# Kernel optimization log

Measured on AMD Instinct MI355X. Metric: run time of the kernel, lower is better.

Reference implementation:

```python
import jax, jax.numpy as jnp
import numpy as np

B, S, H = 4, 1024, 2048
E = 16            # num_experts
K = 2             # num_experts_per_token
I = 1024          # per-expert intermediate_dim
N_SHARED = 2
I_SHARED = I * N_SHARED
RATIO = 0.1       # shared_expert_ratio
EPS = 1e-9


def _swiglu(x, wg, wu, wd):
    # SwiGLU, bias=False: down( silu(gate(x)) * up(x) )
    return (jax.nn.silu(x @ wg) * (x @ wu)) @ wd


def setup_inputs() -> dict:
    key = jax.random.key(0)
    ks = jax.random.split(key, 9)
    scale = 0.02
    x = jax.random.normal(ks[0], (B, S, H), dtype=jnp.float32)
    centroids = jax.random.normal(ks[1], (E, H), dtype=jnp.float32)  # nn.Parameter(randn)
    gate_bias = jnp.zeros((E,), dtype=jnp.float32)
    # shared expert SwiGLU weights (intermediate = I * n_shared_experts)
    wg_s = jax.random.normal(ks[2], (H, I_SHARED), dtype=jnp.float32) * scale
    wu_s = jax.random.normal(ks[3], (H, I_SHARED), dtype=jnp.float32) * scale
    wd_s = jax.random.normal(ks[4], (I_SHARED, H), dtype=jnp.float32) * scale
    # routed experts, stacked [E, ...]
    wg = jax.random.normal(ks[5], (E, H, I), dtype=jnp.float32) * scale
    wu = jax.random.normal(ks[6], (E, H, I), dtype=jnp.float32) * scale
    wd = jax.random.normal(ks[7], (E, I, H), dtype=jnp.float32) * scale
    return {"x": x, "centroids": centroids, "gate_bias": gate_bias,
            "wg_s": wg_s, "wu_s": wu_s, "wd_s": wd_s,
            "wg": wg, "wu": wu, "wd": wd}


def reference(x, centroids, gate_bias, wg_s, wu_s, wd_s, wg, wu, wd):
    # 1) shared expert on ALL tokens, scaled by ratio
    shared = _swiglu(x, wg_s, wu_s, wd_s) * RATIO          # [B,S,H]
    # 2) centroid affinity (DeepSeek-V3 sigmoid gating)
    affinity = jax.nn.sigmoid(jnp.einsum('bsh,eh->bse', x, centroids))  # [B,S,E]
    # 3) bias used ONLY for selection
    biased = affinity + gate_bias
    _, top_idx = jax.lax.top_k(biased, K)                  # [B,S,K]
    # 4) clean weights from unbiased affinity, normalized to sum 1
    top_aff = jnp.take_along_axis(affinity, top_idx, axis=-1)  # [B,S,K]
    weights = top_aff / (top_aff.sum(-1, keepdims=True) + EPS)
    # 5) combine-mask: per-token per-expert weight (0 if not selected)
    mask = (jax.nn.one_hot(top_idx, E, dtype=x.dtype) * weights[..., None]).sum(-2)  # [B,S,E]
    # 6) expert compute + weighted combine; loop over fixed small E avoids
    #    materializing a [B,S,E,H] tensor
    routed = jnp.zeros_like(x)
    for e in range(E):
        routed = routed + mask[..., e:e + 1] * _swiglu(x, wg[e], wu[e], wd[e])
    return shared + routed
```

## Files before the change

kernel.cpp:

```cpp
#include <hip/hip_runtime.h>
#include <hip/hip_bf16.h>

typedef unsigned short u16;
typedef unsigned int u32;
typedef unsigned long long u64;
typedef __attribute__((ext_vector_type(8))) short short8;
typedef __attribute__((ext_vector_type(4))) float f32x4;

#define TOKENS 4096
#define HDIM 2048
#define NEXP 16
#define IDIM 1024
#define ISH 2048
#define MAXT128 80
#define MAXT256 48
#define NCHUNK 128

#define AS1(p) ((const __attribute__((address_space(1))) u32*)(p))
#define AS3(p) ((__attribute__((address_space(3))) u32*)(p))

__device__ __forceinline__ u16 f2b(float f) {
    u32 u = __float_as_uint(f);
    u32 r = u + 0x7fffu + ((u >> 16) & 1u);
    return (u16)(r >> 16);
}

__global__ __launch_bounds__(256) void convert_x_kernel(const float* __restrict__ x,
                                                        u16* __restrict__ xb) {
    size_t i = ((size_t)blockIdx.x * 256 + threadIdx.x) * 8;
    float4 a = *(const float4*)(x + i);
    float4 b = *(const float4*)(x + i + 4);
    u32 p0 = (u32)f2b(a.x) | ((u32)f2b(a.y) << 16);
    u32 p1 = (u32)f2b(a.z) | ((u32)f2b(a.w) << 16);
    u32 p2 = (u32)f2b(b.x) | ((u32)f2b(b.y) << 16);
    u32 p3 = (u32)f2b(b.z) | ((u32)f2b(b.w) << 16);
    uint4 o = make_uint4(p0, p1, p2, p3);
    *(uint4*)(xb + i) = o;
}

__global__ __launch_bounds__(256) void route_kernel(const float* __restrict__ x,
                                                    const float* __restrict__ cent,
                                                    const float* __restrict__ bias,
                                                    int* __restrict__ top_e,
                                                    float* __restrict__ top_w) {
    __shared__ alignas(16) float cs[8 * 2048];
    int lane = threadIdx.x & 63;
    int wv = threadIdx.x >> 6;
    int t = blockIdx.x * 4 + wv;
    const float4* xp4 = (const float4*)(x + (size_t)t * HDIM);
    float4 xr[8];
#pragma unroll
    for (int i = 0; i < 8; i++) xr[i] = xp4[lane + 64 * i];
    float aff[16];
#pragma unroll
    for (int ph = 0; ph < 2; ph++) {
        if (ph) __syncthreads();
        const float* sbase = cent + (size_t)(ph * 8 + wv * 2) * HDIM;
        float* dbase = cs + (size_t)wv * 2 * HDIM;
#pragma unroll
        for (int i = 0; i < 16; i++) {
            __builtin_amdgcn_global_load_lds(AS1(sbase + i * 256 + lane * 4),
                                             AS3(dbase + i * 256), 16, 0, 0);
        }
        __syncthreads();
#pragma unroll
        for (int e = 0; e < 8; e++) {
            const float4* cp = (const float4*)cs + (size_t)e * 512;
            float s = 0.f;
#pragma unroll
            for (int i = 0; i < 8; i++) {
                float4 cv = cp[lane + 64 * i];
                s += xr[i].x * cv.x;
                s += xr[i].y * cv.y;
                s += xr[i].z * cv.z;
                s += xr[i].w * cv.w;
            }
#pragma unroll
            for (int off = 32; off > 0; off >>= 1) s += __shfl_xor(s, off, 64);
            aff[ph * 8 + e] = 1.f / (1.f + expf(-s));
        }
    }
    float b0 = -1e30f, b1 = -1e30f, a0 = 0.f, a1 = 0.f;
    int e0 = -1, e1 = -1;
#pragma unroll
    for (int e = 0; e < 16; e++) {
        float v = aff[e] + bias[e];
        if (v > b0) {
            b1 = b0; e1 = e0; a1 = a0;
            b0 = v; e0 = e; a0 = aff[e];
        } else if (v > b1) {
            b1 = v; e1 = e; a1 = aff[e];
        }
    }
    float inv = 1.f / (a0 + a1 + 1e-9f);
    if (lane == 0) {
        top_e[2 * t] = e0; top_w[2 * t] = a0 * inv;
        top_e[2 * t + 1] = e1; top_w[2 * t + 1] = a1 * inv;
    }
}

__global__ __launch_bounds__(1024) void build_kernel(
    const int* __restrict__ top_e, const float* __restrict__ top_w,
    int* __restrict__ counts, int* __restrict__ offsets,
    int* __restrict__ ntilesA, int* __restrict__ tileA_e, int* __restrict__ tileA_m,
    int* __restrict__ ntilesB, int* __restrict__ tileB_e, int* __restrict__ tileB_m,
    int* __restrict__ list_tok, float* __restrict__ list_w,
    int* __restrict__ tok2slot) {
    __shared__ int cnt[NCHUNK][16];
    __shared__ int offs_s[16];
    __shared__ int totals[16];
    int tid = threadIdx.x;
    int lane = tid & 63, wv = tid >> 6;
    for (int c = wv; c < NCHUNK; c += 16) {
        int v = top_e[c * 64 + lane];
#pragma unroll
        for (int e = 0; e < 16; e++) {
            u64 m = __ballot(v == e);
            if (lane == 0) cnt[c][e] = (int)__popcll(m);
        }
    }
    __syncthreads();
    if (tid < 16) {
        int s = 0;
        for (int c = 0; c < NCHUNK; c++) s += cnt[c][tid];
        totals[tid] = s;
        counts[tid] = s;
    }
    __syncthreads();
    if (tid == 0) {
        int r = 0, ntA = 0, ntB = 0;
        for (int e = 0; e < 16; e++) {
            offs_s[e] = r;
            offsets[e] = r;
            int ce = totals[e];
            int tA = (ce + 127) >> 7;
            for (int m = 0; m < tA; m++) { tileA_e[ntA] = e; tileA_m[ntA] = m; ntA++; }
            int tB = (ce + 255) >> 8;
            for (int m = 0; m < tB; m++) { tileB_e[ntB] = e; tileB_m[ntB] = m; ntB++; }
            r += ce;
        }
        *ntilesA = ntA;
        *ntilesB = ntB;
    }
    __syncthreads();
    if (tid < 16) {
        int r = offs_s[tid];
        for (int c = 0; c < NCHUNK; c++) {
            int v = cnt[c][tid];
            cnt[c][tid] = r;
            r += v;
        }
    }
    __syncthreads();
    for (int c = wv; c < NCHUNK; c += 16) {
        int i = c * 64 + lane;
        int v = top_e[i];
        int rank = 0;
#pragma unroll
        for (int e = 0; e < 16; e++) {
            u64 m = __ballot(v == e);
            if (v == e) rank = (int)__popcll(m & ((1ull << lane) - 1ull));
        }
        int slot = cnt[c][v] + rank;
        list_tok[slot] = i >> 1;
        list_w[slot] = top_w[i];
        tok2slot[i] = slot;
    }
}

__global__ __launch_bounds__(256) void conv_w_kernel(const float* __restrict__ W,
                                                     u16* __restrict__ Wt, int K, int N) {
    int nt = blockIdx.x, kc = blockIdx.y;
    size_t mato = (size_t)blockIdx.z * K * N;
    const float* Wm = W + mato;
    u16* Wtm = Wt + mato;
    int ksB = K >> 5;
    __shared__ u16 Ls[64 * 40];
    int t = threadIdx.x;
    int kr = t >> 3, ng = t & 7;
    int nn = t >> 2, seg = t & 3;
    int g = seg ^ ((nn >> 2) & 3);
#pragma unroll
    for (int s = 0; s < 8; s++) {
        int kb = kc * 256 + s * 32;
        const float* src = Wm + (size_t)(kb + kr) * N + nt * 64 + ng * 8;
        float4 f0 = *(const float4*)src;
        float4 f1 = *(const float4*)(src + 4);
        __syncthreads();
        const float* p0 = (const float*)&f0;
        const float* p1 = (const float*)&f1;
#pragma unroll
        for (int l = 0; l < 4; l++) Ls[(8 * ng + l) * 40 + kr] = f2b(p0[l]);
#pragma unroll
        for (int l = 0; l < 4; l++) Ls[(8 * ng + 4 + l) * 40 + kr] = f2b(p1[l]);
        __syncthreads();
        const u16* lp = &Ls[nn * 40 + g * 8];
        u32 w0 = (u32)lp[0] | ((u32)lp[1] << 16);
        u32 w1 = (u32)lp[2] | ((u32)lp[3] << 16);
        u32 w2 = (u32)lp[4] | ((u32)lp[5] << 16);
        u32 w3 = (u32)lp[6] | ((u32)lp[7] << 16);
        uint4 o = make_uint4(w0, w1, w2, w3);
        *(uint4*)(Wtm + (size_t)(nt * ksB + (kb >> 5)) * 2048 + t * 8) = o;
    }
}

__global__ __launch_bounds__(256) void gemm_gateup(
    const u16* __restrict__ A, const u16* __restrict__ BgAll, const u16* __restrict__ BuAll,
    u16* __restrict__ hout, int Kd, int Nout, const int* __restrict__ counts,
    const int* __restrict__ offsets, const int* __restrict__ ntiles,
    const int* __restrict__ tile_e, const int* __restrict__ tile_m,
    const int* __restrict__ list_tok, int routed) {
    int cnt = TOKENS, base = 0, m0;
    const u16* Bg = BgAll;
    const u16* Bu = BuAll;
    if (routed) {
        int ti = blockIdx.x;
        if (ti >= *ntiles) return;
        int e = tile_e[ti];
        m0 = tile_m[ti] * 128;
        cnt = counts[e];
        base = offsets[e];
        size_t off = (size_t)e * Kd * Nout;
        Bg += off; Bu += off;
    } else {
        m0 = blockIdx.x * 128;
    }
    int nk = Kd >> 6;
    __shared__ alignas(16) u16 As[128 * 64];
    __shared__ alignas(16) u16 Bgs[64 * 64];
    __shared__ alignas(16) u16 Bus[64 * 64];
    int tid = threadIdx.x;
    int lane = tid & 63, wv = tid >> 6;
    int quad = lane >> 4, mr = lane & 15;
    int n0 = blockIdx.y * 64;
    int gk = (tid & 3) ^ ((tid >> 4) & 3);
    int mg0 = min(m0 + (tid >> 2), cnt - 1);
    int mg1 = min(m0 + 64 + (tid >> 2), cnt - 1);
    size_t sr0 = routed ? (size_t)list_tok[base + mg0] : (size_t)mg0;
    size_t sr1 = routed ? (size_t)list_tok[base + mg1] : (size_t)mg1;
    const u16* ap0 = A + sr0 * Kd + gk * 8;
    const u16* ap1 = A + sr1 * Kd + gk * 8;
    size_t bstr = (size_t)(Kd >> 5) * 2048;
    const u16* bgp = Bg + (size_t)blockIdx.y * bstr + tid * 8;
    const u16* bup = Bu + (size_t)blockIdx.y * bstr + tid * 8;
    int xq = quad ^ ((mr >> 2) & 3);
    f32x4 accg[2][4], accu[2][4];
#pragma unroll
    for (int i = 0; i < 2; i++)
#pragma unroll
        for (int j = 0; j < 4; j++) { accg[i][j] = (f32x4)0.f; accu[i][j] = (f32x4)0.f; }

    for (int ks = 0; ks < nk; ks++) {
        __syncthreads();
        __builtin_amdgcn_global_load_lds(AS1(ap0), AS3(As + wv * 512), 16, 0, 0);
        __builtin_amdgcn_global_load_lds(AS1(ap0 + 32), AS3(As + 4096 + wv * 512), 16, 0, 0);
        __builtin_amdgcn_global_load_lds(AS1(ap1), AS3(As + 2048 + wv * 512), 16, 0, 0);
        __builtin_amdgcn_global_load_lds(AS1(ap1 + 32), AS3(As + 6144 + wv * 512), 16, 0, 0);
        __builtin_amdgcn_global_load_lds(AS1(bgp), AS3(Bgs + wv * 512), 16, 0, 0);
        __builtin_amdgcn_global_load_lds(AS1(bgp + 2048), AS3(Bgs + 2048 + wv * 512), 16, 0, 0);
        __builtin_amdgcn_global_load_lds(AS1(bup), AS3(Bus + wv * 512), 16, 0, 0);
        __builtin_amdgcn_global_load_lds(AS1(bup + 2048), AS3(Bus + 2048 + wv * 512), 16, 0, 0);
        ap0 += 64; ap1 += 64; bgp += 4096; bup += 4096;
        __syncthreads();
#pragma unroll
        for (int c = 0; c < 2; c++) {
            short8 a0 = *(const short8*)(As + c * 4096 + ((32 * wv + mr) * 4 + xq) * 8);
            short8 a1 = *(const short8*)(As + c * 4096 + ((32 * wv + 16 + mr) * 4 + xq) * 8);
#pragma unroll
            for (int j = 0; j < 4; j++) {
                short8 bg = *(const short8*)(Bgs + c * 2048 + (64 * j + mr * 4 + xq) * 8);
                short8 bu = *(const short8*)(Bus + c * 2048 + (64 * j + mr * 4 + xq) * 8);
                accg[0][j] = __builtin_amdgcn_mfma_f32_16x16x32_bf16(a0, bg, accg[0][j], 0, 0, 0);
                accg[1][j] = __builtin_amdgcn_mfma_f32_16x16x32_bf16(a1, bg, accg[1][j], 0, 0, 0);
                accu[0][j] = __builtin_amdgcn_mfma_f32_16x16x32_bf16(a0, bu, accu[0][j], 0, 0, 0);
                accu[1][j] = __builtin_amdgcn_mfma_f32_16x16x32_bf16(a1, bu, accu[1][j], 0, 0, 0);
            }
        }
    }
#pragma unroll
    for (int i = 0; i < 2; i++)
#pragma unroll
        for (int j = 0; j < 4; j++)
#pragma unroll
            for (int r = 0; r < 4; r++) {
                int m = m0 + 32 * wv + 16 * i + quad * 4 + r;
                if (m < cnt) {
                    float gv = accg[i][j][r], uv = accu[i][j][r];
                    float h = gv / (1.f + expf(-gv)) * uv;
                    int n = n0 + 16 * j + mr;
                    hout[(size_t)(base + m) * Nout + n] = f2b(h);
                }
            }
}

__global__ __launch_bounds__(256) void gemm_down(
    const u16* __restrict__ A, const u16* __restrict__ BAll, float* __restrict__ outp,
    int Kd, const int* __restrict__ counts, const int* __restrict__ offsets,
    const int* __restrict__ ntiles, const int* __restrict__ tile_e,
    const int* __restrict__ tile_m, const int* __restrict__ list_tok, int routed) {
    int cnt = TOKENS, base = 0, m0;
    const u16* B = BAll;
    if (routed) {
        int ti = blockIdx.x;
        if (ti >= *ntiles) return;
        int e = tile_e[ti];
        m0 = tile_m[ti] * 256;
        cnt = counts[e];
        base = offsets[e];
        B += (size_t)e * Kd * HDIM;
    } else {
        m0 = blockIdx.x * 256;
    }
    int nk = Kd >> 6;
    __shared__ alignas(16) u16 As[256 * 64];
    __shared__ alignas(16) u16 Bs[64 * 64];
    int tid = threadIdx.x;
    int lane = tid & 63, wv = tid >> 6;
    int quad = lane >> 4, mr = lane & 15;
    int n0 = blockIdx.y * 64;
    int gk = (tid & 3) ^ ((tid >> 4) & 3);
    const u16* ap0;
    const u16* ap1;
    const u16* ap2;
    const u16* ap3;
    {
        int mg0 = base + min(m0 + 0 * 64 + (tid >> 2), cnt - 1);
        int mg1 = base + min(m0 + 1 * 64 + (tid >> 2), cnt - 1);
        int mg2 = base + min(m0 + 2 * 64 + (tid >> 2), cnt - 1);
        int mg3 = base + min(m0 + 3 * 64 + (tid >> 2), cnt - 1);
        ap0 = A + (size_t)mg0 * Kd + gk * 8;
        ap1 = A + (size_t)mg1 * Kd + gk * 8;
        ap2 = A + (size_t)mg2 * Kd + gk * 8;
        ap3 = A + (size_t)mg3 * Kd + gk * 8;
    }
    size_t bstr = (size_t)(Kd >> 5) * 2048;
    const u16* bp = B + (size_t)blockIdx.y * bstr + tid * 8;
    int xq = quad ^ ((mr >> 2) & 3);
    f32x4 acc[4][4];
#pragma unroll
    for (int i = 0; i < 4; i++)
#pragma unroll
        for (int j = 0; j < 4; j++) acc[i][j] = (f32x4)0.f;

    for (int ks = 0; ks < nk; ks++) {
        __syncthreads();
        __builtin_amdgcn_global_load_lds(AS1(ap0), AS3(As + 0 + wv * 512), 16, 0, 0);
        __builtin_amdgcn_global_load_lds(AS1(ap0 + 32), AS3(As + 8192 + wv * 512), 16, 0, 0);
        __builtin_amdgcn_global_load_lds(AS1(ap1), AS3(As + 2048 + wv * 512), 16, 0, 0);
        __builtin_amdgcn_global_load_lds(AS1(ap1 + 32), AS3(As + 10240 + wv * 512), 16, 0, 0);
        __builtin_amdgcn_global_load_lds(AS1(ap2), AS3(As + 4096 + wv * 512), 16, 0, 0);
        __builtin_amdgcn_global_load_lds(AS1(ap2 + 32), AS3(As + 12288 + wv * 512), 16, 0, 0);
        __builtin_amdgcn_global_load_lds(AS1(ap3), AS3(As + 6144 + wv * 512), 16, 0, 0);
        __builtin_amdgcn_global_load_lds(AS1(ap3 + 32), AS3(As + 14336 + wv * 512), 16, 0, 0);
        __builtin_amdgcn_global_load_lds(AS1(bp), AS3(Bs + wv * 512), 16, 0, 0);
        __builtin_amdgcn_global_load_lds(AS1(bp + 2048), AS3(Bs + 2048 + wv * 512), 16, 0, 0);
        ap0 += 64; ap1 += 64; ap2 += 64; ap3 += 64; bp += 4096;
        __syncthreads();
#pragma unroll
        for (int c = 0; c < 2; c++) {
            short8 a0 = *(const short8*)(As + c * 8192 + ((64 * wv + 0 + mr) * 4 + xq) * 8);
            short8 a1 = *(const short8*)(As + c * 8192 + ((64 * wv + 16 + mr) * 4 + xq) * 8);
            short8 a2 = *(const short8*)(As + c * 8192 + ((64 * wv + 32 + mr) * 4 + xq) * 8);
            short8 a3 = *(const short8*)(As + c * 8192 + ((64 * wv + 48 + mr) * 4 + xq) * 8);
#pragma unroll
            for (int j = 0; j < 4; j++) {
                short8 b = *(const short8*)(Bs + c * 2048 + (64 * j + mr * 4 + xq) * 8);
                acc[0][j] = __builtin_amdgcn_mfma_f32_16x16x32_bf16(a0, b, acc[0][j], 0, 0, 0);
                acc[1][j] = __builtin_amdgcn_mfma_f32_16x16x32_bf16(a1, b, acc[1][j], 0, 0, 0);
                acc[2][j] = __builtin_amdgcn_mfma_f32_16x16x32_bf16(a2, b, acc[2][j], 0, 0, 0);
                acc[3][j] = __builtin_amdgcn_mfma_f32_16x16x32_bf16(a3, b, acc[3][j], 0, 0, 0);
            }
        }
    }

#pragma unroll
    for (int i = 0; i < 4; i++)
#pragma unroll
        for (int j = 0; j < 4; j++)
#pragma unroll
            for (int r = 0; r < 4; r++) {
                int m = m0 + 64 * wv + 16 * i + quad * 4 + r;
                if (m >= cnt) continue;
                int n = n0 + 16 * j + mr;
                float v = acc[i][j][r];
                if (routed) {
                    outp[(size_t)(base + m) * HDIM + n] = v;
                } else {
                    outp[(size_t)m * HDIM + n] = 0.1f * v;
                }
            }
}

__global__ __launch_bounds__(256) void combine_kernel(float* __restrict__ out,
                                                      const float* __restrict__ rd,
                                                      const int* __restrict__ tok2slot,
                                                      const float* __restrict__ top_w) {
    int t = blockIdx.x;
    int s0 = tok2slot[2 * t], s1 = tok2slot[2 * t + 1];
    float w0 = top_w[2 * t], w1 = top_w[2 * t + 1];
    const float4* r0 = (const float4*)(rd + (size_t)s0 * HDIM);
    const float4* r1 = (const float4*)(rd + (size_t)s1 * HDIM);
    float4* op = (float4*)(out + (size_t)t * HDIM);
#pragma unroll
    for (int k = 0; k < 2; k++) {
        int c = threadIdx.x + k * 256;
        float4 o = op[c];
        float4 a = r0[c];
        float4 b = r1[c];
        o.x += w0 * a.x + w1 * b.x;
        o.y += w0 * a.y + w1 * b.y;
        o.z += w0 * a.z + w1 * b.z;
        o.w += w0 * a.w + w1 * b.w;
        op[c] = o;
    }
}

extern "C" void kernel_launch(void* const* d_in, const int* in_sizes, int n_in,
                              void* d_out, int out_size, void* d_ws, size_t ws_size,
                              hipStream_t stream) {
    const float* x = (const float*)d_in[0];
    const float* cent = (const float*)d_in[1];
    const float* bias = (const float*)d_in[2];
    const float* wgs = (const float*)d_in[3];
    const float* wus = (const float*)d_in[4];
    const float* wds = (const float*)d_in[5];
    const float* wg = (const float*)d_in[6];
    const float* wu = (const float*)d_in[7];
    const float* wd = (const float*)d_in[8];
    float* out = (float*)d_out;
    char* ws = (char*)d_ws;

    size_t off_wtgs = 0;
    size_t off_wtus = off_wtgs + (size_t)HDIM * ISH * 2;
    size_t off_wtds = off_wtus + (size_t)HDIM * ISH * 2;
    size_t off_wtg = off_wtds + (size_t)ISH * HDIM * 2;
    size_t off_wtu = off_wtg + (size_t)NEXP * HDIM * IDIM * 2;
    size_t off_wtd = off_wtu + (size_t)NEXP * HDIM * IDIM * 2;
    size_t off_xbf = off_wtd + (size_t)NEXP * IDIM * HDIM * 2;
    size_t off_hsh = off_xbf + (size_t)TOKENS * HDIM * 2;
    size_t off_hrt = off_hsh + (size_t)TOKENS * ISH * 2;
    size_t off_meta = off_hrt + (size_t)2 * TOKENS * IDIM * 2;
    size_t need = off_meta + (1 << 20);
    if (ws_size < need) return;

    u16* Wt_gs = (u16*)(ws + off_wtgs);
    u16* Wt_us = (u16*)(ws + off_wtus);
    u16* Wt_ds = (u16*)(ws + off_wtds);
    u16* Wt_g = (u16*)(ws + off_wtg);
    u16* Wt_u = (u16*)(ws + off_wtu);
    u16* Wt_d = (u16*)(ws + off_wtd);
    u16* x_bf = (u16*)(ws + off_xbf);
    u16* h_sh = (u16*)(ws + off_hsh);
    u16* h_rt = (u16*)(ws + off_hrt);
    float* rd = (float*)ws;
    int* counts = (int*)(ws + off_meta);
    int* offsets = counts + 16;
    int* ntilesA = offsets + 16;
    int* ntilesB = ntilesA + 8;
    int* tileA_e = ntilesB + 8;
    int* tileA_m = tileA_e + MAXT128;
    int* tileB_e = tileA_m + MAXT128;
    int* tileB_m = tileB_e + MAXT256;
    int* tok2slot = tileB_m + MAXT256;
    int* top_e = tok2slot + 2 * TOKENS;
    float* top_w = (float*)(top_e + 2 * TOKENS);
    int* list_tok = (int*)(top_w + 2 * TOKENS);
    float* list_w = (float*)(list_tok + 2 * TOKENS);

    convert_x_kernel<<<TOKENS * HDIM / (256 * 8), 256, 0, stream>>>(x, x_bf);
    route_kernel<<<TOKENS / 4, 256, 0, stream>>>(x, cent, bias, top_e, top_w);
    build_kernel<<<1, 1024, 0, stream>>>(top_e, top_w, counts, offsets, ntilesA, tileA_e,
                                         tileA_m, ntilesB, tileB_e, tileB_m, list_tok,
                                         list_w, tok2slot);

    conv_w_kernel<<<dim3(ISH / 64, HDIM / 256, 1), 256, 0, stream>>>(wgs, Wt_gs, HDIM, ISH);
    conv_w_kernel<<<dim3(ISH / 64, HDIM / 256, 1), 256, 0, stream>>>(wus, Wt_us, HDIM, ISH);
    conv_w_kernel<<<dim3(HDIM / 64, ISH / 256, 1), 256, 0, stream>>>(wds, Wt_ds, ISH, HDIM);
    conv_w_kernel<<<dim3(IDIM / 64, HDIM / 256, NEXP), 256, 0, stream>>>(wg, Wt_g, HDIM, IDIM);
    conv_w_kernel<<<dim3(IDIM / 64, HDIM / 256, NEXP), 256, 0, stream>>>(wu, Wt_u, HDIM, IDIM);
    conv_w_kernel<<<dim3(HDIM / 64, IDIM / 256, NEXP), 256, 0, stream>>>(wd, Wt_d, IDIM, HDIM);

    gemm_gateup<<<dim3(TOKENS / 128, ISH / 64, 1), 256, 0, stream>>>(
        x_bf, Wt_gs, Wt_us, h_sh, HDIM, ISH, nullptr, nullptr, nullptr, nullptr, nullptr,
        nullptr, 0);
    gemm_down<<<dim3(TOKENS / 256, HDIM / 64, 1), 256, 0, stream>>>(
        h_sh, Wt_ds, out, ISH, nullptr, nullptr, nullptr, nullptr, nullptr, nullptr, 0);
    gemm_gateup<<<dim3(MAXT128, IDIM / 64, 1), 256, 0, stream>>>(
        x_bf, Wt_g, Wt_u, h_rt, HDIM, IDIM, counts, offsets, ntilesA, tileA_e, tileA_m,
        list_tok, 1);
    gemm_down<<<dim3(MAXT256, HDIM / 64, 1), 256, 0, stream>>>(
        h_rt, Wt_d, rd, IDIM, counts, offsets, ntilesB, tileB_e, tileB_m, list_tok, 1);
    combine_kernel<<<TOKENS, 256, 0, stream>>>(out, rd, tok2slot, top_w);
}
```

Before: 884.0 us.

## Merge shared and routed expert GEMMs into single launches with swizzled work-item lists

The build kernel now emits flat work-item lists for gate/up and down. Each list covers both the shared-expert tiles and the per-expert routed tiles, grouped into 4x4 blocks of (m, n) tiles. Each GEMM kernel decodes its item through an index remap based on blockIdx&7, so tiles that reuse the same data are meant to land on the same XCD and L2. This replaces two launches per stage and the serial tail of the smaller routed grids, and it merges paired weight-conversion launches. The routed output buffer moves into the routed gate/up weight region so it does not overlap weights the merged down kernel still reads; the cost is extra item decoding and early-exit blocks for padding items.

```diff
diff --git a/kernel.cpp b/kernel.cpp
--- a/kernel.cpp
+++ b/kernel.cpp
@@ -12,9 +12,12 @@
 #define NEXP 16
 #define IDIM 1024
 #define ISH 2048
-#define MAXT128 80
-#define MAXT256 48
 #define NCHUNK 128
+
+#define GUITEMS 2304
+#define GUCHUNK 288
+#define DITEMS 2048
+#define DCHUNK 256
 
 #define AS1(p) ((const __attribute__((address_space(1))) u32*)(p))
 #define AS3(p) ((__attribute__((address_space(3))) u32*)(p))
@@ -101,16 +104,16 @@
 
 __global__ __launch_bounds__(1024) void build_kernel(
     const int* __restrict__ top_e, const float* __restrict__ top_w,
-    int* __restrict__ counts, int* __restrict__ offsets,
-    int* __restrict__ ntilesA, int* __restrict__ tileA_e, int* __restrict__ tileA_m,
-    int* __restrict__ ntilesB, int* __restrict__ tileB_e, int* __restrict__ tileB_m,
-    int* __restrict__ list_tok, float* __restrict__ list_w,
-    int* __restrict__ tok2slot) {
+    int* __restrict__ counts, int* __restrict__ offsets, int* __restrict__ itemsGU,
+    int* __restrict__ itemsD, int* __restrict__ list_tok, int* __restrict__ tok2slot) {
     __shared__ int cnt[NCHUNK][16];
     __shared__ int offs_s[16];
     __shared__ int totals[16];
+    __shared__ int guPref[16], dPref[16];
     int tid = threadIdx.x;
     int lane = tid & 63, wv = tid >> 6;
+    for (int i = tid; i < GUITEMS; i += 1024) itemsGU[i] = -1;
+    for (int i = tid; i < DITEMS; i += 1024) itemsD[i] = -1;
     for (int c = wv; c < NCHUNK; c += 16) {
         int v = top_e[c * 64 + lane];
 #pragma unroll
@@ -128,26 +131,48 @@
     }
     __syncthreads();
     if (tid == 0) {
-        int r = 0, ntA = 0, ntB = 0;
+        int r = 0, g = 0, d = 0;
         for (int e = 0; e < 16; e++) {
             offs_s[e] = r;
             offsets[e] = r;
-            int ce = totals[e];
-            int tA = (ce + 127) >> 7;
-            for (int m = 0; m < tA; m++) { tileA_e[ntA] = e; tileA_m[ntA] = m; ntA++; }
-            int tB = (ce + 255) >> 8;
-            for (int m = 0; m < tB; m++) { tileB_e[ntB] = e; tileB_m[ntB] = m; ntB++; }
-            r += ce;
-        }
-        *ntilesA = ntA;
-        *ntilesB = ntB;
+            r += totals[e];
+            guPref[e] = g;
+            g += ((totals[e] + 127) >> 7) * 16;
+            dPref[e] = d;
+            d += ((totals[e] + 255) >> 8) * 32;
+        }
+    }
+    {
+        int i = tid;
+        int g = i >> 4, s = i & 15;
+        int y0 = (g >> 3) << 2, m0 = (g & 7) << 2;
+        itemsGU[i] = ((m0 + (s >> 2)) << 8) | (y0 + (s & 3));
+    }
+    if (tid < 512) {
+        int i = tid;
+        int g = i >> 4, s = i & 15;
+        int y0 = (g >> 2) << 2, m0 = (g & 3) << 2;
+        itemsD[i] = ((m0 + (s >> 2)) << 8) | (y0 + (s & 3));
     }
     __syncthreads();
     if (tid < 16) {
-        int r = offs_s[tid];
+        int e = tid;
+        int tA = (totals[e] + 127) >> 7;
+        int p = 1024 + guPref[e];
+        for (int y0 = 0; y0 < 16; y0 += 4)
+            for (int m = 0; m < tA; m++)
+                for (int dy = 0; dy < 4; dy++)
+                    itemsGU[p++] = (1 << 28) | (e << 20) | (m << 8) | (y0 + dy);
+        int tB = (totals[e] + 255) >> 8;
+        p = 512 + dPref[e];
+        for (int y0 = 0; y0 < 32; y0 += 4)
+            for (int m = 0; m < tB; m++)
+                for (int dy = 0; dy < 4; dy++)
+                    itemsD[p++] = (1 << 28) | (e << 20) | (m << 8) | (y0 + dy);
+        int r = offs_s[e];
         for (int c = 0; c < NCHUNK; c++) {
-            int v = cnt[c][tid];
-            cnt[c][tid] = r;
+            int v = cnt[c][e];
+            cnt[c][e] = r;
             r += v;
         }
     }
@@ -163,17 +188,27 @@
         }
         int slot = cnt[c][v] + rank;
         list_tok[slot] = i >> 1;
-        list_w[slot] = top_w[i];
         tok2slot[i] = slot;
     }
 }
 
 __global__ __launch_bounds__(256) void conv_w_kernel(const float* __restrict__ W,
-                                                     u16* __restrict__ Wt, int K, int N) {
+                                                     const float* __restrict__ W2,
+                                                     u16* __restrict__ Wt,
+                                                     u16* __restrict__ Wt2, int K, int N,
+                                                     int zsplit) {
     int nt = blockIdx.x, kc = blockIdx.y;
-    size_t mato = (size_t)blockIdx.z * K * N;
-    const float* Wm = W + mato;
-    u16* Wtm = Wt + mato;
+    int zz = blockIdx.z;
+    const float* Wm;
+    u16* Wtm;
+    if (zz < zsplit) {
+        Wm = W + (size_t)zz * K * N;
+        Wtm = Wt + (size_t)zz * K * N;
+    } else {
+        int z2 = zz - zsplit;
+        Wm = W2 + (size_t)z2 * K * N;
+        Wtm = Wt2 + (size_t)z2 * K * N;
+    }
     int ksB = K >> 5;
     __shared__ u16 Ls[64 * 40];
     int t = threadIdx.x;
@@ -205,44 +240,54 @@
 }
 
 __global__ __launch_bounds__(256) void gemm_gateup(
-    const u16* __restrict__ A, const u16* __restrict__ BgAll, const u16* __restrict__ BuAll,
-    u16* __restrict__ hout, int Kd, int Nout, const int* __restrict__ counts,
-    const int* __restrict__ offsets, const int* __restrict__ ntiles,
-    const int* __restrict__ tile_e, const int* __restrict__ tile_m,
-    const int* __restrict__ list_tok, int routed) {
-    int cnt = TOKENS, base = 0, m0;
-    const u16* Bg = BgAll;
-    const u16* Bu = BuAll;
+    const u16* __restrict__ A, const u16* __restrict__ BgS, const u16* __restrict__ BuS,
+    const u16* __restrict__ BgR, const u16* __restrict__ BuR, u16* __restrict__ hS,
+    u16* __restrict__ hR, const int* __restrict__ counts, const int* __restrict__ offsets,
+    const int* __restrict__ list_tok, const int* __restrict__ items) {
+    int idx = (blockIdx.x & 7) * GUCHUNK + (blockIdx.x >> 3);
+    int it = items[idx];
+    if (it < 0) return;
+    int routed = (it >> 28) & 1;
+    int e = (it >> 20) & 15;
+    int m0 = ((it >> 8) & 4095) * 128;
+    int yb = it & 255;
+    int cnt, base, Nout;
+    const u16 *Bg, *Bu;
+    u16* hout;
     if (routed) {
-        int ti = blockIdx.x;
-        if (ti >= *ntiles) return;
-        int e = tile_e[ti];
-        m0 = tile_m[ti] * 128;
         cnt = counts[e];
         base = offsets[e];
-        size_t off = (size_t)e * Kd * Nout;
-        Bg += off; Bu += off;
+        Nout = IDIM;
+        size_t off = (size_t)e * HDIM * IDIM;
+        Bg = BgR + off;
+        Bu = BuR + off;
+        hout = hR;
     } else {
-        m0 = blockIdx.x * 128;
-    }
-    int nk = Kd >> 6;
+        cnt = TOKENS;
+        base = 0;
+        Nout = ISH;
+        Bg = BgS;
+        Bu = BuS;
+        hout = hS;
+    }
+    const int nk = HDIM >> 6;
     __shared__ alignas(16) u16 As[128 * 64];
     __shared__ alignas(16) u16 Bgs[64 * 64];
     __shared__ alignas(16) u16 Bus[64 * 64];
     int tid = threadIdx.x;
     int lane = tid & 63, wv = tid >> 6;
     int quad = lane >> 4, mr = lane & 15;
-    int n0 = blockIdx.y * 64;
+    int n0 = yb * 64;
     int gk = (tid & 3) ^ ((tid >> 4) & 3);
     int mg0 = min(m0 + (tid >> 2), cnt - 1);
     int mg1 = min(m0 + 64 + (tid >> 2), cnt - 1);
     size_t sr0 = routed ? (size_t)list_tok[base + mg0] : (size_t)mg0;
     size_t sr1 = routed ? (size_t)list_tok[base + mg1] : (size_t)mg1;
-    const u16* ap0 = A + sr0 * Kd + gk * 8;
-    const u16* ap1 = A + sr1 * Kd + gk * 8;
-    size_t bstr = (size_t)(Kd >> 5) * 2048;
-    const u16* bgp = Bg + (size_t)blockIdx.y * bstr + tid * 8;
-    const u16* bup = Bu + (size_t)blockIdx.y * bstr + tid * 8;
+    const u16* ap0 = A + sr0 * HDIM + gk * 8;
+    const u16* ap1 = A + sr1 * HDIM + gk * 8;
+    size_t bstr = (size_t)(HDIM >> 5) * 2048;
+    const u16* bgp = Bg + (size_t)yb * bstr + tid * 8;
+    const u16* bup = Bu + (size_t)yb * bstr + tid * 8;
     int xq = quad ^ ((mr >> 2) & 3);
     f32x4 accg[2][4], accu[2][4];
 #pragma unroll
@@ -294,22 +339,34 @@
 }
 
 __global__ __launch_bounds__(256) void gemm_down(
-    const u16* __restrict__ A, const u16* __restrict__ BAll, float* __restrict__ outp,
-    int Kd, const int* __restrict__ counts, const int* __restrict__ offsets,
-    const int* __restrict__ ntiles, const int* __restrict__ tile_e,
-    const int* __restrict__ tile_m, const int* __restrict__ list_tok, int routed) {
-    int cnt = TOKENS, base = 0, m0;
-    const u16* B = BAll;
+    const u16* __restrict__ hS, const u16* __restrict__ hR, const u16* __restrict__ BdS,
+    const u16* __restrict__ BdR, float* __restrict__ out, float* __restrict__ rd,
+    const int* __restrict__ counts, const int* __restrict__ offsets,
+    const int* __restrict__ items) {
+    int idx = (blockIdx.x & 7) * DCHUNK + (blockIdx.x >> 3);
+    int it = items[idx];
+    if (it < 0) return;
+    int routed = (it >> 28) & 1;
+    int e = (it >> 20) & 15;
+    int m0 = ((it >> 8) & 4095) * 256;
+    int yb = it & 255;
+    int cnt, base, Kd;
+    const u16 *A, *B;
+    float* outp;
     if (routed) {
-        int ti = blockIdx.x;
-        if (ti >= *ntiles) return;
-        int e = tile_e[ti];
-        m0 = tile_m[ti] * 256;
         cnt = counts[e];
         base = offsets[e];
-        B += (size_t)e * Kd * HDIM;
+        Kd = IDIM;
+        A = hR;
+        B = BdR + (size_t)e * IDIM * HDIM;
+        outp = rd;
     } else {
-        m0 = blockIdx.x * 256;
+        cnt = TOKENS;
+        base = 0;
+        Kd = ISH;
+        A = hS;
+        B = BdS;
+        outp = out;
     }
     int nk = Kd >> 6;
     __shared__ alignas(16) u16 As[256 * 64];
@@ -317,7 +374,7 @@
     int tid = threadIdx.x;
     int lane = tid & 63, wv = tid >> 6;
     int quad = lane >> 4, mr = lane & 15;
-    int n0 = blockIdx.y * 64;
+    int n0 = yb * 64;
     int gk = (tid & 3) ^ ((tid >> 4) & 3);
     const u16* ap0;
     const u16* ap1;
@@ -334,7 +391,7 @@
         ap3 = A + (size_t)mg3 * Kd + gk * 8;
     }
     size_t bstr = (size_t)(Kd >> 5) * 2048;
-    const u16* bp = B + (size_t)blockIdx.y * bstr + tid * 8;
+    const u16* bp = B + (size_t)yb * bstr + tid * 8;
     int xq = quad ^ ((mr >> 2) & 3);
     f32x4 acc[4][4];
 #pragma unroll
@@ -452,43 +509,33 @@
     u16* x_bf = (u16*)(ws + off_xbf);
     u16* h_sh = (u16*)(ws + off_hsh);
     u16* h_rt = (u16*)(ws + off_hrt);
-    float* rd = (float*)ws;
+    float* rd = (float*)(ws + off_wtg);
     int* counts = (int*)(ws + off_meta);
     int* offsets = counts + 16;
-    int* ntilesA = offsets + 16;
-    int* ntilesB = ntilesA + 8;
-    int* tileA_e = ntilesB + 8;
-    int* tileA_m = tileA_e + MAXT128;
-    int* tileB_e = tileA_m + MAXT128;
-    int* tileB_m = tileB_e + MAXT256;
-    int* tok2slot = tileB_m + MAXT256;
+    int* itemsGU = offsets + 16;
+    int* itemsD = itemsGU + GUITEMS;
+    int* tok2slot = itemsD + DITEMS;
     int* top_e = tok2slot + 2 * TOKENS;
     float* top_w = (float*)(top_e + 2 * TOKENS);
     int* list_tok = (int*)(top_w + 2 * TOKENS);
-    float* list_w = (float*)(list_tok + 2 * TOKENS);
 
     convert_x_kernel<<<TOKENS * HDIM / (256 * 8), 256, 0, stream>>>(x, x_bf);
     route_kernel<<<TOKENS / 4, 256, 0, stream>>>(x, cent, bias, top_e, top_w);
-    build_kernel<<<1, 1024, 0, stream>>>(top_e, top_w, counts, offsets, ntilesA, tileA_e,
-                                         tileA_m, ntilesB, tileB_e, tileB_m, list_tok,
-                                         list_w, tok2slot);
-
-    conv_w_kernel<<<dim3(ISH / 64, HDIM / 256, 1), 256, 0, stream>>>(wgs, Wt_gs, HDIM, ISH);
-    conv_w_kernel<<<dim3(ISH / 64, HDIM / 256, 1), 256, 0, stream>>>(wus, Wt_us, HDIM, ISH);
-    conv_w_kernel<<<dim3(HDIM / 64, ISH / 256, 1), 256, 0, stream>>>(wds, Wt_ds, ISH, HDIM);
-    conv_w_kernel<<<dim3(IDIM / 64, HDIM / 256, NEXP), 256, 0, stream>>>(wg, Wt_g, HDIM, IDIM);
-    conv_w_kernel<<<dim3(IDIM / 64, HDIM / 256, NEXP), 256, 0, stream>>>(wu, Wt_u, HDIM, IDIM);
-    conv_w_kernel<<<dim3(HDIM / 64, IDIM / 256, NEXP), 256, 0, stream>>>(wd, Wt_d, IDIM, HDIM);
-
-    gemm_gateup<<<dim3(TOKENS / 128, ISH / 64, 1), 256, 0, stream>>>(
-        x_bf, Wt_gs, Wt_us, h_sh, HDIM, ISH, nullptr, nullptr, nullptr, nullptr, nullptr,
-        nullptr, 0);
-    gemm_down<<<dim3(TOKENS / 256, HDIM / 64, 1), 256, 0, stream>>>(
-        h_sh, Wt_ds, out, ISH, nullptr, nullptr, nullptr, nullptr, nullptr, nullptr, 0);
-    gemm_gateup<<<dim3(MAXT128, IDIM / 64, 1), 256, 0, stream>>>(
-        x_bf, Wt_g, Wt_u, h_rt, HDIM, IDIM, counts, offsets, ntilesA, tileA_e, tileA_m,
-        list_tok, 1);
-    gemm_down<<<dim3(MAXT256, HDIM / 64, 1), 256, 0, stream>>>(
-        h_rt, Wt_d, rd, IDIM, counts, offsets, ntilesB, tileB_e, tileB_m, list_tok, 1);
+    build_kernel<<<1, 1024, 0, stream>>>(top_e, top_w, counts, offsets, itemsGU, itemsD,
+                                         list_tok, tok2slot);
+
+    conv_w_kernel<<<dim3(ISH / 64, HDIM / 256, 2), 256, 0, stream>>>(
+        wgs, wus, Wt_gs, Wt_us, HDIM, ISH, 1);
+    conv_w_kernel<<<dim3(HDIM / 64, ISH / 256, 1), 256, 0, stream>>>(
+        wds, wds, Wt_ds, Wt_ds, ISH, HDIM, 1);
+    conv_w_kernel<<<dim3(IDIM / 64, HDIM / 256, 2 * NEXP), 256, 0, stream>>>(
+        wg, wu, Wt_g, Wt_u, HDIM, IDIM, NEXP);
+    conv_w_kernel<<<dim3(HDIM / 64, IDIM / 256, NEXP), 256, 0, stream>>>(
+        wd, wd, Wt_d, Wt_d, IDIM, HDIM, NEXP);
+
+    gemm_gateup<<<GUITEMS, 256, 0, stream>>>(x_bf, Wt_gs, Wt_us, Wt_g, Wt_u, h_sh, h_rt,
+                                             counts, offsets, list_tok, itemsGU);
+    gemm_down<<<DITEMS, 256, 0, stream>>>(h_sh, h_rt, Wt_ds, Wt_d, out, rd, counts,
+                                          offsets, itemsD);
     combine_kernel<<<TOKENS, 256, 0, stream>>>(out, rd, tok2slot, top_w);
 }
```

Result: slower. 927.6 us (+4.9%).
